# Performance work log

Hardware: AMD Instinct MI355X
Metric: run time of the kernel (lower is better)

## Reference

```python
import jax, jax.numpy as jnp
import numpy as np

D_MODEL = 1024
N_HEADS = 16
D_K = D_MODEL // N_HEADS
D_FF = 4096
EPS = 1e-5


def setup_inputs() -> dict:
    key = jax.random.key(0)
    ks = jax.random.split(key, 12)
    s = 1.0 / np.sqrt(D_MODEL)
    inp = {
        "x": jax.random.normal(ks[0], (2, 2048, D_MODEL), dtype=jnp.float32),
        "Wq": jax.random.normal(ks[1], (D_MODEL, D_MODEL), dtype=jnp.float32) * s,
        "Wk": jax.random.normal(ks[2], (D_MODEL, D_MODEL), dtype=jnp.float32) * s,
        "Wv": jax.random.normal(ks[3], (D_MODEL, D_MODEL), dtype=jnp.float32) * s,
        "Wo": jax.random.normal(ks[4], (D_MODEL, D_MODEL), dtype=jnp.float32) * s,
        "ln1_g": jnp.ones((D_MODEL,), jnp.float32),
        "ln1_b": jnp.zeros((D_MODEL,), jnp.float32),
        "ln2_g": jnp.ones((D_MODEL,), jnp.float32),
        "ln2_b": jnp.zeros((D_MODEL,), jnp.float32),
        "W1": jax.random.normal(ks[5], (D_MODEL, D_FF), dtype=jnp.float32) * s,
        "b1": jnp.zeros((D_FF,), jnp.float32),
        "W2": jax.random.normal(ks[6], (D_FF, D_MODEL), dtype=jnp.float32) * (1.0 / np.sqrt(D_FF)),
        "b2": jnp.zeros((D_MODEL,), jnp.float32),
    }
    return inp


def _layernorm(x, g, b):
    mu = jnp.mean(x, axis=-1, keepdims=True)
    var = jnp.mean(jnp.square(x - mu), axis=-1, keepdims=True)
    return (x - mu) / jnp.sqrt(var + EPS) * g + b


def _mha(x, Wq, Wk, Wv, Wo):
    B, S, D = x.shape
    def split_heads(t):
        return t.reshape(B, S, N_HEADS, D_K).transpose(0, 2, 1, 3)  # [B,H,S,Dk]
    Q = split_heads(x @ Wq)
    K = split_heads(x @ Wk)
    V = split_heads(x @ Wv)
    scores = jnp.einsum("bhsd,bhtd->bhst", Q, K) / np.sqrt(D_K)
    causal = jnp.tril(jnp.ones((S, S), dtype=bool))
    scores = jnp.where(causal, scores, -jnp.inf)
    weights = jax.nn.softmax(scores, axis=-1)
    out = jnp.einsum("bhst,bhtd->bhsd", weights, V)
    out = out.transpose(0, 2, 1, 3).reshape(B, S, D)
    return out @ Wo


def reference(x, Wq, Wk, Wv, Wo, ln1_g, ln1_b, ln2_g, ln2_b, W1, b1, W2, b2):
    # Pre-LN transformer block, dropout in eval mode (identity)
    x = x + _mha(_layernorm(x, ln1_g, ln1_b), Wq, Wk, Wv, Wo)
    h = _layernorm(x, ln2_g, ln2_b)
    ff = jax.nn.gelu(h @ W1 + b1, approximate=False) @ W2 + b2
    return x + ff
```

## Files before the change

### kernel.cpp

```cpp
#include <hip/hip_runtime.h>
#include <cstdint>
#include <cstddef>

#define DEV __device__ __forceinline__

typedef __attribute__((ext_vector_type(8))) __bf16 bf16x8;
typedef __attribute__((ext_vector_type(4))) float f32x4;
typedef __attribute__((ext_vector_type(8))) unsigned short u16x8;

typedef const __attribute__((address_space(1))) void gld_gv;
typedef __attribute__((address_space(3))) void gld_sv;

static constexpr int SEQ = 2048, BAT = 2, DM = 1024, DFF = 4096;
static constexpr int MT = BAT * SEQ;
static constexpr float LOG2E = 1.44269504088896340736f;

DEV unsigned short f2bf_bits(float f) {
    uint32_t u = __builtin_bit_cast(uint32_t, f);
    return (unsigned short)((u + 0x7FFFu + ((u >> 16) & 1u)) >> 16);
}

DEV void gload16(const void* g, void* s) {
    __builtin_amdgcn_global_load_lds((gld_gv*)g, (gld_sv*)s, 16, 0, 0);
}

__global__ __launch_bounds__(256) void wtrans_kernel(const float* __restrict__ W,
        unsigned short* __restrict__ WT, int K, int N, float scale)
{
    __shared__ float tile[64][65];
    const int k0 = blockIdx.x * 64, n0 = blockIdx.y * 64;
    const int t = threadIdx.x, r = t >> 6, c = t & 63;
    #pragma unroll
    for (int p = 0; p < 16; ++p)
        tile[p * 4 + r][c] = W[(size_t)(k0 + p * 4 + r) * N + n0 + c];
    __syncthreads();
    #pragma unroll
    for (int p = 0; p < 16; ++p)
        WT[(size_t)(n0 + p * 4 + r) * K + k0 + c] = f2bf_bits(tile[c][p * 4 + r] * scale);
}

__global__ __launch_bounds__(256) void ln_kernel(const float* __restrict__ x,
        const float* __restrict__ gw, const float* __restrict__ bw,
        unsigned short* __restrict__ y)
{
    const int row = blockIdx.x, t = threadIdx.x;
    const float* xr = x + (size_t)row * DM;
    float4 v = *(const float4*)(xr + t * 4);
    float s = v.x + v.y + v.z + v.w;
    float q = v.x * v.x + v.y * v.y + v.z * v.z + v.w * v.w;
    #pragma unroll
    for (int m = 1; m < 64; m <<= 1) { s += __shfl_xor(s, m); q += __shfl_xor(q, m); }
    __shared__ float red[8];
    const int w = t >> 6;
    if ((t & 63) == 0) { red[w] = s; red[4 + w] = q; }
    __syncthreads();
    s = red[0] + red[1] + red[2] + red[3];
    q = red[4] + red[5] + red[6] + red[7];
    const float mu = s * (1.0f / DM);
    const float rstd = rsqrtf(q * (1.0f / DM) - mu * mu + 1e-5f);
    float4 g4 = *(const float4*)(gw + t * 4);
    float4 b4 = *(const float4*)(bw + t * 4);
    short4 o;
    o.x = (short)f2bf_bits((v.x - mu) * rstd * g4.x + b4.x);
    o.y = (short)f2bf_bits((v.y - mu) * rstd * g4.y + b4.y);
    o.z = (short)f2bf_bits((v.z - mu) * rstd * g4.z + b4.z);
    o.w = (short)f2bf_bits((v.w - mu) * rstd * g4.w + b4.w);
    *(short4*)(y + (size_t)row * DM + t * 4) = o;
}

template<int EPI, int BM, int BN, int WVM, int WVN>
__global__ __launch_bounds__(WVM * WVN * 64, (BN == 64 ? 3 : 2)) void gemm_pipe(
    const unsigned short* __restrict__ A, const unsigned short* __restrict__ BT,
    void* __restrict__ Cp, const float* __restrict__ bias,
    const float* __restrict__ res, int Nsz, int Ksz, float scale)
{
    constexpr int NT = WVM * WVN * 64;
    constexpr int TOTCH = (BM + BN) * 8;
    constexpr int TL = TOTCH / NT;
    constexpr int MREP = BM / (WVM * 16);
    constexpr int WMR = MREP * 16;
    __shared__ alignas(16) unsigned short lds[2][(BM + BN) * 64];

    const int t = threadIdx.x, l = t & 63, w = t >> 6;
    const int wm = w / WVN, wn = w % WVN;
    const int lr = l & 15, lg = l >> 4;
    const int bm = blockIdx.x, bn = blockIdx.y;

    f32x4 acc[MREP][4] = {};

    const int nk = Ksz / 64;

    auto STAGE = [&](int tile, char* slot) {
        const int k0 = tile * 64;
        #pragma unroll
        for (int p = 0; p < TL; ++p) {
            const int ci = t + p * NT;
            const bool isA = ci < BM * 8;
            const int rr = (isA ? ci : ci - BM * 8) >> 3;
            const int cc = ci & 7;
            const unsigned short* srow = isA
                ? A + (size_t)(bm * BM + rr) * Ksz
                : BT + (size_t)(bn * BN + rr) * Ksz;
            gload16(srow + k0 + ((cc ^ (rr & 7)) << 3), slot + ci * 16);
        }
    };

    STAGE(0, (char*)lds[0]);
    STAGE(1, (char*)lds[1]);

    for (int kt = 0; kt < nk; ++kt) {
        char* slot = (char*)lds[kt & 1];
        const char* la = slot;
        const char* lb = slot + BM * 128;
        if (kt + 1 < nk) {
            if constexpr (TL == 8) asm volatile("s_waitcnt vmcnt(8)" ::: "memory");
            else                   asm volatile("s_waitcnt vmcnt(6)" ::: "memory");
        } else {
            asm volatile("s_waitcnt vmcnt(0)" ::: "memory");
        }
        __builtin_amdgcn_s_barrier();
        __builtin_amdgcn_sched_barrier(0);

        __builtin_amdgcn_s_setprio(1);
        #pragma unroll
        for (int ks = 0; ks < 2; ++ks) {
            bf16x8 af[MREP], bfr[4];
            #pragma unroll
            for (int i = 0; i < MREP; ++i) {
                const int ra = wm * WMR + i * 16 + lr;
                af[i] = *(const bf16x8*)(la + (ra * 8 + ((ks * 4 + lg) ^ (ra & 7))) * 16);
            }
            #pragma unroll
            for (int i = 0; i < 4; ++i) {
                const int rb_ = wn * 64 + i * 16 + lr;
                bfr[i] = *(const bf16x8*)(lb + (rb_ * 8 + ((ks * 4 + lg) ^ (rb_ & 7))) * 16);
            }
            #pragma unroll
            for (int mb = 0; mb < MREP; ++mb)
                #pragma unroll
                for (int nb = 0; nb < 4; ++nb) {
                    if (EPI == 4)
                        acc[mb][nb] = __builtin_amdgcn_mfma_f32_16x16x32_bf16(
                            bfr[nb], af[mb], acc[mb][nb], 0, 0, 0);
                    else
                        acc[mb][nb] = __builtin_amdgcn_mfma_f32_16x16x32_bf16(
                            af[mb], bfr[nb], acc[mb][nb], 0, 0, 0);
                }
        }
        __builtin_amdgcn_s_setprio(0);
        __builtin_amdgcn_s_barrier();
        if (kt + 2 < nk) STAGE(kt + 2, slot);
    }

    const int rb = bm * BM + wm * WMR, cb = bn * BN + wn * 64;
    #pragma unroll
    for (int mb = 0; mb < MREP; ++mb)
        #pragma unroll
        for (int nb = 0; nb < 4; ++nb)
            #pragma unroll
            for (int r = 0; r < 4; ++r) {
                float v = acc[mb][nb][r];
                if (EPI == 4) {
                    const int xrow = rb + mb * 16 + lr;
                    const int feat = cb + nb * 16 + lg * 4 + r;
                    const int bb = xrow >> 11, s = xrow & (SEQ - 1);
                    ((unsigned short*)Cp)[((size_t)bb * DM + feat) * SEQ + s] = f2bf_bits(v);
                    continue;
                }
                const int row = rb + mb * 16 + lg * 4 + r;
                const int col = cb + nb * 16 + lr;
                const size_t idx = (size_t)row * Nsz + col;
                if (EPI == 0) {
                    ((unsigned short*)Cp)[idx] = f2bf_bits(v * scale);
                } else if (EPI == 1) {
                    ((float*)Cp)[idx] = v + res[idx];
                } else if (EPI == 2) {
                    float xx = v + bias[col];
                    ((unsigned short*)Cp)[idx] =
                        f2bf_bits(0.5f * xx * (1.0f + erff(xx * 0.70710678118654752f)));
                } else {
                    ((float*)Cp)[idx] = v + bias[col] + res[idx];
                }
            }
}

__global__ __launch_bounds__(512, 2) void attn_kernel(
    const unsigned short* __restrict__ QKg, const unsigned short* __restrict__ VTg,
    unsigned short* __restrict__ Og)
{
    __shared__ alignas(16) unsigned short ldsK[2][128 * 64];
    __shared__ alignas(16) unsigned short ldsVT[2][64 * 128];
    const int t = threadIdx.x, l = t & 63, w = t >> 6;
    const int lr = l & 15, lg = l >> 4;
    const int qtA = blockIdx.x, qtB = 15 - qtA;
    const int bh = blockIdx.y;
    const int b = bh >> 4, h = bh & 15;
    const unsigned short* Qbase = QKg + (size_t)b * SEQ * 2048 + h * 64;
    const unsigned short* Kbase = Qbase + 1024;
    const unsigned short* Vbase = VTg + (size_t)b * DM * SEQ + (size_t)(h * 64) * SEQ;

    const int wq0A = qtA * 128 + w * 16, qrowA = wq0A + lr;
    const int wq0B = qtB * 128 + w * 16, qrowB = wq0B + lr;
    bf16x8 qfA[2], qfB[2];
    #pragma unroll
    for (int ks = 0; ks < 2; ++ks) {
        qfA[ks] = *(const bf16x8*)(Qbase + (size_t)qrowA * 2048 + ks * 32 + lg * 8);
        qfB[ks] = *(const bf16x8*)(Qbase + (size_t)qrowB * 2048 + ks * 32 + lg * 8);
    }

    float m_runA = -1e30f, l_partA = 0.0f;
    float m_runB = -1e30f, l_partB = 0.0f;
    f32x4 oaccA[4] = {}, oaccB[4] = {};

    const int kci[2] = { t, t + 512 };
    const int nkt = qtB + 1;

    #pragma unroll
    for (int p = 0; p < 2; ++p) {
        const int ci = kci[p];
        const int kr = ci >> 3, kc = (ci & 7) ^ (kr & 7);
        gload16(Kbase + (size_t)kr * 2048 + kc * 8, (char*)ldsK[0] + ci * 16);
        const int vr = ci >> 4, vc = (ci & 15) ^ (vr & 15);
        gload16(Vbase + (size_t)vr * SEQ + vc * 8, (char*)ldsVT[0] + ci * 16);
    }
    asm volatile("s_waitcnt vmcnt(0)" ::: "memory");
    __builtin_amdgcn_s_barrier();

    for (int kt = 0; kt < nkt; ++kt) {
        const int cur = kt & 1;
        if (kt + 1 < nkt) {
            #pragma unroll
            for (int p = 0; p < 2; ++p) {
                const int ci = kci[p];
                const int kr = ci >> 3, kc = (ci & 7) ^ (kr & 7);
                gload16(Kbase + (size_t)((kt + 1) * 128 + kr) * 2048 + kc * 8,
                        (char*)ldsK[cur ^ 1] + ci * 16);
                const int vr = ci >> 4, vc = (ci & 15) ^ (vr & 15);
                gload16(Vbase + (size_t)vr * SEQ + (kt + 1) * 128 + vc * 8,
                        (char*)ldsVT[cur ^ 1] + ci * 16);
            }
        }
        const char* lk = (const char*)ldsK[cur];
        const char* lv = (const char*)ldsVT[cur];

        auto process = [&](const bf16x8 (&qf)[2], f32x4 (&oacc)[4],
                           float& m_run, float& l_part, int qrow, bool diag) {
            __builtin_amdgcn_s_setprio(1);
            f32x4 st[8] = {};
            #pragma unroll
            for (int ks = 0; ks < 2; ++ks)
                #pragma unroll
                for (int mb = 0; mb < 8; ++mb) {
                    bf16x8 kf = *(const bf16x8*)(lk + (mb * 16 + lr) * 128
                                                 + (((ks * 4 + lg) ^ (lr & 7)) * 16));
                    st[mb] = __builtin_amdgcn_mfma_f32_16x16x32_bf16(kf, qf[ks], st[mb], 0, 0, 0);
                }
            __builtin_amdgcn_s_setprio(0);

            const int kt0 = kt * 128;
            if (diag) {
                #pragma unroll
                for (int mb = 0; mb < 8; ++mb)
                    #pragma unroll
                    for (int r = 0; r < 4; ++r)
                        if (kt0 + mb * 16 + lg * 4 + r > qrow) st[mb][r] = -1e30f;
            }

            f32x4 mx4 = st[0];
            #pragma unroll
            for (int mb = 1; mb < 8; ++mb) {
                mx4[0] = fmaxf(mx4[0], st[mb][0]); mx4[1] = fmaxf(mx4[1], st[mb][1]);
                mx4[2] = fmaxf(mx4[2], st[mb][2]); mx4[3] = fmaxf(mx4[3], st[mb][3]);
            }
            const float mt = fmaxf(fmaxf(mx4[0], mx4[1]), fmaxf(mx4[2], mx4[3]));

            if (!__all(mt <= m_run + 8.0f)) {
                float mr = fmaxf(mt, __shfl_xor(mt, 16));
                mr = fmaxf(mr, __shfl_xor(mr, 32));
                const float m_new = fmaxf(m_run, mr);
                const float alpha = exp2f((m_run - m_new) * LOG2E);
                l_part *= alpha;
                #pragma unroll
                for (int j = 0; j < 4; ++j) {
                    const float aj = __shfl(alpha, lg * 4 + j);
                    #pragma unroll
                    for (int nb = 0; nb < 4; ++nb) oacc[nb][j] *= aj;
                }
                m_run = m_new;
            }

            const float nml = m_run * LOG2E;
            float rsl = 0.0f;
            #pragma unroll
            for (int mb = 0; mb < 8; ++mb)
                #pragma unroll
                for (int r = 0; r < 4; ++r) {
                    const float p = exp2f(fmaf(st[mb][r], LOG2E, -nml));
                    st[mb][r] = p;
                    rsl += p;
                }
            l_part += rsl;

            bf16x8 pa[4];
            #pragma unroll
            for (int ks = 0; ks < 4; ++ks)
                #pragma unroll
                for (int j = 0; j < 4; ++j) {
                    pa[ks][j]     = (__bf16)st[2 * ks][j];
                    pa[ks][j + 4] = (__bf16)st[2 * ks + 1][j];
                }

            __builtin_amdgcn_s_setprio(1);
            #pragma unroll
            for (int ks = 0; ks < 4; ++ks)
                #pragma unroll
                for (int nb = 0; nb < 4; ++nb) {
                    const int n = nb * 16 + lr;
                    union { bf16x8 v; uint64_t d[2]; } vb;
                    vb.d[0] = *(const uint64_t*)(lv + n * 256
                                + (((4 * ks + (lg >> 1)) ^ (n & 15)) * 16) + 8 * (lg & 1));
                    vb.d[1] = *(const uint64_t*)(lv + n * 256
                                + (((4 * ks + 2 + (lg >> 1)) ^ (n & 15)) * 16) + 8 * (lg & 1));
                    oacc[nb] = __builtin_amdgcn_mfma_f32_16x16x32_bf16(pa[ks], vb.v, oacc[nb], 0, 0, 0);
                }
            __builtin_amdgcn_s_setprio(0);
        };

        if (kt <= qtA) process(qfA, oaccA, m_runA, l_partA, qrowA, kt == qtA);
        process(qfB, oaccB, m_runB, l_partB, qrowB, kt == qtB);

        asm volatile("s_waitcnt vmcnt(0)" ::: "memory");
        __builtin_amdgcn_s_barrier();
    }

    unsigned short* Obase = Og + (size_t)b * SEQ * DM + h * 64;
    {
        float lr_ = l_partA;
        lr_ += __shfl_xor(lr_, 16); lr_ += __shfl_xor(lr_, 32);
        #pragma unroll
        for (int j = 0; j < 4; ++j) {
            const float inv = 1.0f / __shfl(lr_, lg * 4 + j);
            const int row = wq0A + lg * 4 + j;
            #pragma unroll
            for (int nb = 0; nb < 4; ++nb)
                Obase[(size_t)row * DM + nb * 16 + lr] = f2bf_bits(oaccA[nb][j] * inv);
        }
    }
    {
        float lr_ = l_partB;
        lr_ += __shfl_xor(lr_, 16); lr_ += __shfl_xor(lr_, 32);
        #pragma unroll
        for (int j = 0; j < 4; ++j) {
            const float inv = 1.0f / __shfl(lr_, lg * 4 + j);
            const int row = wq0B + lg * 4 + j;
            #pragma unroll
            for (int nb = 0; nb < 4; ++nb)
                Obase[(size_t)row * DM + nb * 16 + lr] = f2bf_bits(oaccB[nb][j] * inv);
        }
    }
}

extern "C" void kernel_launch(void* const* d_in, const int* in_sizes, int n_in,
                              void* d_out, int out_size, void* d_ws, size_t ws_size,
                              hipStream_t stream) {
    (void)in_sizes; (void)n_in; (void)out_size; (void)ws_size;
    const float* x    = (const float*)d_in[0];
    const float* Wq   = (const float*)d_in[1];
    const float* Wk   = (const float*)d_in[2];
    const float* Wv   = (const float*)d_in[3];
    const float* Wo   = (const float*)d_in[4];
    const float* ln1g = (const float*)d_in[5];
    const float* ln1b = (const float*)d_in[6];
    const float* ln2g = (const float*)d_in[7];
    const float* ln2b = (const float*)d_in[8];
    const float* W1   = (const float*)d_in[9];
    const float* b1   = (const float*)d_in[10];
    const float* W2   = (const float*)d_in[11];
    const float* b2   = (const float*)d_in[12];
    float* out = (float*)d_out;

    char* ws = (char*)d_ws;
    const size_t MB = 1ull << 20;
    unsigned short* xn1   = (unsigned short*)(ws + 0 * MB);
    unsigned short* QKb   = (unsigned short*)(ws + 8 * MB);
    unsigned short* VTg   = (unsigned short*)(ws + 24 * MB);
    unsigned short* ffa   = (unsigned short*)(ws + 0 * MB);
    unsigned short* attno = (unsigned short*)(ws + 32 * MB);
    float*          x2    = (float*)(ws + 40 * MB);
    unsigned short* h2    = (unsigned short*)(ws + 56 * MB);
    unsigned short* WqkT  = (unsigned short*)(ws + 64 * MB);
    unsigned short* WvT   = (unsigned short*)(ws + 68 * MB);
    unsigned short* WoT   = (unsigned short*)(ws + 70 * MB);
    unsigned short* W1T   = (unsigned short*)(ws + 72 * MB);
    unsigned short* W2T   = (unsigned short*)(ws + 80 * MB);

    dim3 blk(256);
    wtrans_kernel<<<dim3(16, 16), blk, 0, stream>>>(Wq, WqkT, DM, DM, 0.125f);
    wtrans_kernel<<<dim3(16, 16), blk, 0, stream>>>(Wk, WqkT + DM * DM, DM, DM, 1.0f);
    wtrans_kernel<<<dim3(16, 16), blk, 0, stream>>>(Wv, WvT, DM, DM, 1.0f);
    wtrans_kernel<<<dim3(16, 16), blk, 0, stream>>>(Wo, WoT, DM, DM, 1.0f);
    wtrans_kernel<<<dim3(16, 64), blk, 0, stream>>>(W1, W1T, DM, DFF, 1.0f);
    wtrans_kernel<<<dim3(64, 16), blk, 0, stream>>>(W2, W2T, DFF, DM, 1.0f);

    ln_kernel<<<dim3(MT), blk, 0, stream>>>(x, ln1g, ln1b, xn1);

    gemm_pipe<0, 128, 256, 2, 4><<<dim3(32, 8), dim3(512), 0, stream>>>(
        xn1, WqkT, QKb, nullptr, nullptr, 2048, DM, 1.0f);
    gemm_pipe<4, 128, 64, 4, 1><<<dim3(32, 16), blk, 0, stream>>>(
        xn1, WvT, VTg, nullptr, nullptr, DM, DM, 1.0f);

    attn_kernel<<<dim3(8, 32), dim3(512), 0, stream>>>(QKb, VTg, attno);

    gemm_pipe<1, 128, 64, 4, 1><<<dim3(32, 16), blk, 0, stream>>>(
        attno, WoT, x2, nullptr, x, DM, DM, 1.0f);

    ln_kernel<<<dim3(MT), blk, 0, stream>>>(x2, ln2g, ln2b, h2);

    gemm_pipe<2, 128, 128, 2, 2><<<dim3(32, 32), blk, 0, stream>>>(
        h2, W1T, ffa, b1, nullptr, DFF, DM, 1.0f);
    gemm_pipe<3, 128, 64, 4, 1><<<dim3(32, 16), blk, 0, stream>>>(
        ffa, W2T, out, b2, x2, DM, DFF, 1.0f);
}
```

Before: 243.0 us.

## Add 256x256 eight-wave GEMM with phased LDS staging for FFN up-projection

Introduces a new GEMM kernel with 256x256 output tiles, 8 waves, and a K loop split into four phases, with MFMA priority raised during compute. Global-to-LDS loads for the next tiles are interleaved between the phases using partial vmcnt waits, so that memory traffic overlaps MFMA work. The W1 GEMM with bias+GELU epilogue now uses this kernel on a 16x16 grid instead of 128x128 tiles on a 32x32 grid. This raises data reuse per block, but the grid has only 256 blocks and each thread keeps 128 accumulator floats, which increases register pressure and could reduce occupancy.

Measured after the change: 241.1 us. No clear change (-0.8%).

```diff
diff --git a/kernel.cpp b/kernel.cpp
--- a/kernel.cpp
+++ b/kernel.cpp
@@ -178,6 +178,122 @@
                     float xx = v + bias[col];
                     ((unsigned short*)Cp)[idx] =
                         f2bf_bits(0.5f * xx * (1.0f + erff(xx * 0.70710678118654752f)));
+                } else {
+                    ((float*)Cp)[idx] = v + bias[col] + res[idx];
+                }
+            }
+}
+
+template<int P>
+DEV void phase8_mfma(const char* base, int wm, int lr, int lg,
+                     const bf16x8 (&bfr)[2][4], f32x4 (&acc)[8][4]) {
+    bf16x8 af[2][2];
+    #pragma unroll
+    for (int ks = 0; ks < 2; ++ks)
+        #pragma unroll
+        for (int m = 0; m < 2; ++m) {
+            const int ra = wm * 128 + P * 32 + m * 16 + lr;
+            af[ks][m] = *(const bf16x8*)(base + (ra * 8 + ((ks * 4 + lg) ^ (ra & 7))) * 16);
+        }
+    __builtin_amdgcn_s_barrier();
+    __builtin_amdgcn_s_setprio(1);
+    #pragma unroll
+    for (int ks = 0; ks < 2; ++ks)
+        #pragma unroll
+        for (int m = 0; m < 2; ++m)
+            #pragma unroll
+            for (int nb = 0; nb < 4; ++nb)
+                acc[P * 2 + m][nb] = __builtin_amdgcn_mfma_f32_16x16x32_bf16(
+                    af[ks][m], bfr[ks][nb], acc[P * 2 + m][nb], 0, 0, 0);
+    __builtin_amdgcn_s_setprio(0);
+}
+
+template<int EPI>
+__global__ __launch_bounds__(512, 2) void gemm_8ph(
+    const unsigned short* __restrict__ A, const unsigned short* __restrict__ BT,
+    void* __restrict__ Cp, const float* __restrict__ bias,
+    const float* __restrict__ res, int Nsz, int Ksz, float scale)
+{
+    __shared__ alignas(16) unsigned short lds[2][32768];
+    const int t = threadIdx.x, l = t & 63, w = t >> 6;
+    const int wm = w >> 2, wn = w & 3;
+    const int lr = l & 15, lg = l >> 4;
+    const int bm = blockIdx.x, bn = blockIdx.y;
+
+    f32x4 acc[8][4] = {};
+    const int nk = Ksz / 64;
+
+    const unsigned short* Ab = A + (size_t)(bm * 256) * Ksz;
+    const unsigned short* Bb = BT + (size_t)(bn * 256) * Ksz;
+
+    auto stage = [&](int tile, int region) {
+        char* base = (char*)lds[tile & 1];
+        const int k0 = tile * 64;
+        #pragma unroll
+        for (int j = 0; j < 2; ++j) {
+            const int ci = t + j * 512;
+            const int rr = ci >> 3, c = ci & 7;
+            int row; const unsigned short* src; int dchunk;
+            if (region == 0)      { row = rr;                          src = Bb; dchunk = 2048 + row * 8 + c; }
+            else if (region == 1) { row = 128 + rr;                    src = Bb; dchunk = 2048 + row * 8 + c; }
+            else if (region == 2) { row = (rr < 64 ? rr : rr + 64);    src = Ab; dchunk = row * 8 + c; }
+            else                  { row = 64 + (rr < 64 ? rr : rr + 64); src = Ab; dchunk = row * 8 + c; }
+            gload16(src + (size_t)row * Ksz + k0 + ((c ^ (row & 7)) << 3),
+                    base + dchunk * 16);
+        }
+    };
+
+    stage(0, 0); stage(0, 1); stage(0, 2); stage(0, 3);
+    stage(1, 0); stage(1, 1); stage(1, 2);
+    asm volatile("s_waitcnt vmcnt(6)" ::: "memory");
+    __builtin_amdgcn_s_barrier();
+    __builtin_amdgcn_sched_barrier(0);
+
+    bf16x8 bfr[2][4];
+    for (int kt = 0; kt < nk; ++kt) {
+        const char* base = (const char*)lds[kt & 1];
+        if (kt + 1 < nk) stage(kt + 1, 3);
+        #pragma unroll
+        for (int ks = 0; ks < 2; ++ks)
+            #pragma unroll
+            for (int nb = 0; nb < 4; ++nb) {
+                const int rb_ = wn * 64 + nb * 16 + lr;
+                bfr[ks][nb] = *(const bf16x8*)(base
+                    + (2048 + rb_ * 8 + ((ks * 4 + lg) ^ (rb_ & 7))) * 16);
+            }
+        phase8_mfma<0>(base, wm, lr, lg, bfr, acc);
+        __builtin_amdgcn_s_barrier();
+        if (kt + 2 < nk) stage(kt + 2, 0);
+        phase8_mfma<1>(base, wm, lr, lg, bfr, acc);
+        __builtin_amdgcn_s_barrier();
+        if (kt + 2 < nk) stage(kt + 2, 1);
+        phase8_mfma<2>(base, wm, lr, lg, bfr, acc);
+        __builtin_amdgcn_s_barrier();
+        if (kt + 2 < nk) stage(kt + 2, 2);
+        phase8_mfma<3>(base, wm, lr, lg, bfr, acc);
+        if (kt + 2 < nk) asm volatile("s_waitcnt vmcnt(6)" ::: "memory");
+        else             asm volatile("s_waitcnt vmcnt(0)" ::: "memory");
+        __builtin_amdgcn_s_barrier();
+        __builtin_amdgcn_sched_barrier(0);
+    }
+
+    const int rb = bm * 256 + wm * 128, cb = bn * 256 + wn * 64;
+    #pragma unroll
+    for (int mb = 0; mb < 8; ++mb)
+        #pragma unroll
+        for (int nb = 0; nb < 4; ++nb)
+            #pragma unroll
+            for (int r = 0; r < 4; ++r) {
+                float v = acc[mb][nb][r];
+                const int row = rb + mb * 16 + lg * 4 + r;
+                const int col = cb + nb * 16 + lr;
+                const size_t idx = (size_t)row * Nsz + col;
+                if (EPI == 2) {
+                    float xx = v + bias[col];
+                    ((unsigned short*)Cp)[idx] =
+                        f2bf_bits(0.5f * xx * (1.0f + erff(xx * 0.70710678118654752f)));
+                } else if (EPI == 0) {
+                    ((unsigned short*)Cp)[idx] = f2bf_bits(v * scale);
                 } else {
                     ((float*)Cp)[idx] = v + bias[col] + res[idx];
                 }
@@ -416,7 +532,7 @@
 
     ln_kernel<<<dim3(MT), blk, 0, stream>>>(x2, ln2g, ln2b, h2);
 
-    gemm_pipe<2, 128, 128, 2, 2><<<dim3(32, 32), blk, 0, stream>>>(
+    gemm_8ph<2><<<dim3(16, 16), dim3(512), 0, stream>>>(
         h2, W1T, ffa, b1, nullptr, DFF, DM, 1.0f);
     gemm_pipe<3, 128, 64, 4, 1><<<dim3(32, 16), blk, 0, stream>>>(
         ffa, W2T, out, b2, x2, DM, DFF, 1.0f);
```
